# Performance work log

Measured on AMD Instinct MI355X. Metric: run time of the kernel, lower is better.

## Reference

```python
import jax, jax.numpy as jnp
import numpy as np

N = 4096
IN_F = 512
OUT_F = 256
HEADS = 4
HEAD_DIM = OUT_F // HEADS


def setup_inputs() -> dict:
    key = jax.random.key(0)
    k_feat, k_adj, k_w, k_a = jax.random.split(key, 4)
    features = jax.random.normal(k_feat, (N, IN_F), dtype=jnp.float32)
    adj_matrix = jax.random.uniform(k_adj, (N, N), dtype=jnp.float32)
    # xavier-uniform-ish init scaled small
    W = jax.random.normal(k_w, (OUT_F, IN_F), dtype=jnp.float32) * (1.0 / np.sqrt(IN_F))
    a = jax.random.normal(k_a, (HEADS, 2 * HEAD_DIM), dtype=jnp.float32) * 0.1
    bias = jnp.zeros((OUT_F,), dtype=jnp.float32)
    return {"features": features, "adj_matrix": adj_matrix, "W": W, "a": a, "bias": bias}


def reference(features, adj_matrix, W, a, bias):
    n = features.shape[0]
    h = features @ W.T                      # [N, OUT_F]
    hh = h.reshape(n, HEADS, HEAD_DIM)      # [N, H, D]
    # e[i,j,h] = leaky_relu(<h_i, a[:, :D]> + <h_j, a[:, D:]>) -- additive decomposition
    e_src = jnp.einsum('nhd,hd->nh', hh, a[:, :HEAD_DIM])   # [N, H]
    e_dst = jnp.einsum('nhd,hd->nh', hh, a[:, HEAD_DIM:])   # [N, H]
    e = e_src[:, None, :] + e_dst[None, :, :]               # [N, N, H]
    e = jnp.where(e >= 0, e, 0.2 * e)                       # leaky_relu(0.2)
    mask = adj_matrix[:, :, None] > 0.1                     # [N, N, 1]
    e = jnp.where(mask, e, -jnp.inf)
    attention = jax.nn.softmax(e, axis=1)                   # softmax over j
    attention = jnp.nan_to_num(attention, nan=0.0)          # fully-masked rows -> 0
    attention_mean = attention.mean(axis=2)                 # [N, N]
    h_out = attention_mean @ h + bias                       # [N, OUT_F]
    return h_out
```

## Files before the change

### kernel.cpp

```cpp
#include <hip/hip_runtime.h>
#include <math.h>

#define NN      4096
#define INF_    512
#define OUTF    256
#define NHEAD   4
#define HDIM    64
#define KSPLIT  16

typedef __attribute__((ext_vector_type(8))) short  short8x;
typedef __attribute__((ext_vector_type(4))) float  float4x;

__device__ __forceinline__ unsigned short f2bf(float x) {
    union { float f; unsigned int u; } c; c.f = x;
    unsigned int r = (c.u + 0x7FFFu + ((c.u >> 16) & 1u)) >> 16;
    return (unsigned short)r;
}
__device__ __forceinline__ float bflo(unsigned int u) {
    union { unsigned int x; float f; } c; c.x = u << 16; return c.f;
}
__device__ __forceinline__ float bfhi(unsigned int u) {
    union { unsigned int x; float f; } c; c.x = u & 0xFFFF0000u; return c.f;
}

__global__ __launch_bounds__(256) void k_cast(const float* __restrict__ feat,
                                              const float* __restrict__ W,
                                              unsigned short* __restrict__ featb,
                                              unsigned short* __restrict__ Wb) {
    const int b = blockIdx.x;
    const float* src;
    unsigned short* dst;
    int idx;
    if (b < 2048) { src = feat; dst = featb; idx = b * 1024 + threadIdx.x * 4; }
    else          { src = W;    dst = Wb;    idx = (b - 2048) * 1024 + threadIdx.x * 4; }
    float4x v = *(const float4x*)(src + idx);
    ushort4 u;
    u.x = f2bf(v[0]); u.y = f2bf(v[1]); u.z = f2bf(v[2]); u.w = f2bf(v[3]);
    *(ushort4*)(dst + idx) = u;
}

__global__ __launch_bounds__(256) void k_hedge(const unsigned short* __restrict__ featb,
                                               const unsigned short* __restrict__ Wb,
                                               const float* __restrict__ a,
                                               unsigned short* __restrict__ hT,
                                               float* __restrict__ es,
                                               unsigned short* __restrict__ Bt,
                                               unsigned short* __restrict__ Dt) {
    __shared__ __align__(16) unsigned short lds_f[16 * 40];
    __shared__ __align__(16) unsigned short lds_w[256 * 40];
    const int tid  = threadIdx.x;
    const int w    = tid >> 6;
    const int lane = tid & 63;
    const int lidx = lane & 15;
    const int quad = lane >> 4;
    const int i0   = blockIdx.x * 16;
    const int fr = (tid & 127) >> 3;
    const int fk = (tid & 7) * 4;
    const int wr = tid >> 3;
    const int wk = (tid & 7) * 4;

    float4x acc[4];
    #pragma unroll
    for (int nt = 0; nt < 4; ++nt) acc[nt] = (float4x){0.f, 0.f, 0.f, 0.f};

    ushort4 pf{0,0,0,0};
    ushort4 pw[8];
    if (tid < 128)
        pf = *(const ushort4*)&featb[(size_t)(i0 + fr) * INF_ + fk];
    #pragma unroll
    for (int it = 0; it < 8; ++it)
        pw[it] = *(const ushort4*)&Wb[(size_t)(it * 32 + wr) * INF_ + wk];

    for (int kt = 0; kt < INF_; kt += 32) {
        __syncthreads();
        if (tid < 128)
            *(ushort4*)&lds_f[fr * 40 + fk] = pf;
        #pragma unroll
        for (int it = 0; it < 8; ++it)
            *(ushort4*)&lds_w[(it * 32 + wr) * 40 + wk] = pw[it];
        __syncthreads();
        if (kt + 32 < INF_) {
            const int kn = kt + 32;
            if (tid < 128)
                pf = *(const ushort4*)&featb[(size_t)(i0 + fr) * INF_ + kn + fk];
            #pragma unroll
            for (int it = 0; it < 8; ++it)
                pw[it] = *(const ushort4*)&Wb[(size_t)(it * 32 + wr) * INF_ + kn + wk];
        }
        short8x af = *(const short8x*)&lds_f[lidx * 40 + quad * 8];
        short8x bw[4];
        #pragma unroll
        for (int nt = 0; nt < 4; ++nt)
            bw[nt] = *(const short8x*)&lds_w[(w * 64 + nt * 16 + lidx) * 40 + quad * 8];
        #pragma unroll
        for (int nt = 0; nt < 4; ++nt)
            acc[nt] = __builtin_amdgcn_mfma_f32_16x16x32_bf16(af, bw[nt], acc[nt], 0, 0, 0);
    }
    #pragma unroll
    for (int nt = 0; nt < 4; ++nt) {
        int col = w * 64 + nt * 16 + lidx;
        int m0r = i0 + quad * 4;
        ushort4 u;
        u.x = f2bf(acc[nt][0]); u.y = f2bf(acc[nt][1]);
        u.z = f2bf(acc[nt][2]); u.w = f2bf(acc[nt][3]);
        *(ushort4*)&hT[(size_t)col * NN + m0r] = u;
    }
    float asrc[4], adst[4];
    #pragma unroll
    for (int nt = 0; nt < 4; ++nt) {
        asrc[nt] = a[w * 2 * HDIM + nt * 16 + lidx];
        adst[nt] = a[w * 2 * HDIM + HDIM + nt * 16 + lidx];
    }
    #pragma unroll
    for (int r = 0; r < 4; ++r) {
        float s = 0.f, d = 0.f;
        #pragma unroll
        for (int nt = 0; nt < 4; ++nt) {
            s += acc[nt][r] * asrc[nt];
            d += acc[nt][r] * adst[nt];
        }
        #pragma unroll
        for (int off = 1; off < 16; off <<= 1) {
            s += __shfl_xor(s, off);
            d += __shfl_xor(d, off);
        }
        if (lidx == 0) {
            int row = i0 + quad * 4 + r;
            es[row * NHEAD + w] = s;
            Bt[row * NHEAD + w] = f2bf(__expf(d));
            Dt[row * NHEAD + w] = f2bf(__expf(0.2f * d));
        }
    }
}

__global__ __launch_bounds__(256) void k_attn(const float* __restrict__ adj,
                                              const float* __restrict__ es,
                                              const unsigned short* __restrict__ Bt,
                                              const unsigned short* __restrict__ Dt,
                                              unsigned short* __restrict__ attn) {
    __shared__ float red[4][8];
    __shared__ float cfs[8];
    const int tid = threadIdx.x;
    const int wv  = tid >> 6;
    const int lane = tid & 63;
    const int i = blockIdx.x;

    const float4x esv = ((const float4x*)es)[i];
    float TB[4];
    #pragma unroll
    for (int h = 0; h < 4; ++h) TB[h] = __expf(-esv[h]);
    const float4x* arow4 = (const float4x*)(adj + (size_t)i * NN);
    const uint4* B4 = (const uint4*)Bt;
    const uint4* D4 = (const uint4*)Dt;

    float4x av[4];
    float S1[4] = {0.f, 0.f, 0.f, 0.f};
    float S2[4] = {0.f, 0.f, 0.f, 0.f};
    #pragma unroll
    for (int t = 0; t < 4; ++t) {
        int jv = t * 256 + tid;
        av[t] = arow4[jv];
        uint4 bu0 = B4[jv * 2], bu1 = B4[jv * 2 + 1];
        uint4 du0 = D4[jv * 2], du1 = D4[jv * 2 + 1];
        unsigned int bwv[8] = {bu0.x, bu0.y, bu0.z, bu0.w, bu1.x, bu1.y, bu1.z, bu1.w};
        unsigned int dwv[8] = {du0.x, du0.y, du0.z, du0.w, du1.x, du1.y, du1.z, du1.w};
        #pragma unroll
        for (int u = 0; u < 4; ++u) {
            bool m = av[t][u] > 0.1f;
            float b0 = bflo(bwv[u * 2]), b1 = bfhi(bwv[u * 2]);
            float b2 = bflo(bwv[u * 2 + 1]), b3 = bfhi(bwv[u * 2 + 1]);
            float d0 = bflo(dwv[u * 2]), d1 = bfhi(dwv[u * 2]);
            float d2 = bflo(dwv[u * 2 + 1]), d3 = bfhi(dwv[u * 2 + 1]);
            bool p0 = b0 >= TB[0], p1 = b1 >= TB[1], p2 = b2 >= TB[2], p3 = b3 >= TB[3];
            S1[0] += (m && p0) ? b0 : 0.f;   S2[0] += (m && !p0) ? d0 : 0.f;
            S1[1] += (m && p1) ? b1 : 0.f;   S2[1] += (m && !p1) ? d1 : 0.f;
            S1[2] += (m && p2) ? b2 : 0.f;   S2[2] += (m && !p2) ? d2 : 0.f;
            S1[3] += (m && p3) ? b3 : 0.f;   S2[3] += (m && !p3) ? d3 : 0.f;
        }
    }
    #pragma unroll
    for (int off = 1; off < 64; off <<= 1) {
        #pragma unroll
        for (int h = 0; h < 4; ++h) {
            S1[h] += __shfl_xor(S1[h], off);
            S2[h] += __shfl_xor(S2[h], off);
        }
    }
    if (lane == 0) {
        #pragma unroll
        for (int h = 0; h < 4; ++h) { red[wv][h] = S1[h]; red[wv][4 + h] = S2[h]; }
    }
    __syncthreads();
    if (tid < 8)
        cfs[tid] = red[0][tid] + red[1][tid] + red[2][tid] + red[3][tid];
    __syncthreads();
    float cA[4], cC[4];
    #pragma unroll
    for (int h = 0; h < 4; ++h) {
        float A = __expf(esv[h]), C = __expf(0.2f * esv[h]);
        float den = A * cfs[h] + C * cfs[4 + h];
        float sc = den > 0.f ? 0.25f / den : 0.f;
        cA[h] = A * sc;
        cC[h] = C * sc;
    }

    unsigned short* orow = attn + (size_t)i * NN;
    #pragma unroll
    for (int t = 0; t < 4; ++t) {
        int jv = t * 256 + tid;
        uint4 bu0 = B4[jv * 2], bu1 = B4[jv * 2 + 1];
        uint4 du0 = D4[jv * 2], du1 = D4[jv * 2 + 1];
        unsigned int bwv[8] = {bu0.x, bu0.y, bu0.z, bu0.w, bu1.x, bu1.y, bu1.z, bu1.w};
        unsigned int dwv[8] = {du0.x, du0.y, du0.z, du0.w, du1.x, du1.y, du1.z, du1.w};
        ushort4 o;
        unsigned short* op = (unsigned short*)&o;
        #pragma unroll
        for (int u = 0; u < 4; ++u) {
            float b0 = bflo(bwv[u * 2]), b1 = bfhi(bwv[u * 2]);
            float b2 = bflo(bwv[u * 2 + 1]), b3 = bfhi(bwv[u * 2 + 1]);
            float d0 = bflo(dwv[u * 2]), d1 = bfhi(dwv[u * 2]);
            float d2 = bflo(dwv[u * 2 + 1]), d3 = bfhi(dwv[u * 2 + 1]);
            float p;
            p  = (b0 >= TB[0]) ? cA[0] * b0 : cC[0] * d0;
            p += (b1 >= TB[1]) ? cA[1] * b1 : cC[1] * d1;
            p += (b2 >= TB[2]) ? cA[2] * b2 : cC[2] * d2;
            p += (b3 >= TB[3]) ? cA[3] * b3 : cC[3] * d3;
            op[u] = f2bf((av[t][u] > 0.1f) ? p : 0.f);
        }
        *(ushort4*)&orow[jv * 4] = o;
    }
}

__global__ __launch_bounds__(256) void k_out_gemm(const unsigned short* __restrict__ attn,
                                                  const unsigned short* __restrict__ hT,
                                                  float* __restrict__ partials) {
    __shared__ __align__(16) unsigned short lds_a[64 * 40];
    __shared__ __align__(16) unsigned short lds_h[256 * 40];
    const int tid  = threadIdx.x;
    const int w    = tid >> 6;
    const int lane = tid & 63;
    const int lidx = lane & 15;
    const int quad = lane >> 4;
    const int i0    = blockIdx.x * 64;
    const int kbase = blockIdx.y * (NN / KSPLIT);
    const int srow = tid >> 3;
    const int skq  = tid & 7;

    float4x acc[4][4];
    #pragma unroll
    for (int p = 0; p < 4; ++p)
        #pragma unroll
        for (int q = 0; q < 4; ++q)
            acc[p][q] = (float4x){0.f, 0.f, 0.f, 0.f};

    ushort4 pa[2], ph[8];
    #pragma unroll
    for (int it = 0; it < 2; ++it)
        pa[it] = *(const ushort4*)&attn[(size_t)(i0 + it * 32 + srow) * NN + kbase + skq * 4];
    #pragma unroll
    for (int it = 0; it < 8; ++it)
        ph[it] = *(const ushort4*)&hT[(size_t)(it * 32 + srow) * NN + kbase + skq * 4];

    const int KSTEPS = (NN / KSPLIT) / 32;
    for (int ks = 0; ks < KSTEPS; ++ks) {
        __syncthreads();
        #pragma unroll
        for (int it = 0; it < 2; ++it)
            *(ushort4*)&lds_a[(it * 32 + srow) * 40 + skq * 4] = pa[it];
        #pragma unroll
        for (int it = 0; it < 8; ++it)
            *(ushort4*)&lds_h[(it * 32 + srow) * 40 + skq * 4] = ph[it];
        __syncthreads();
        if (ks < KSTEPS - 1) {
            const int ktn = kbase + (ks + 1) * 32;
            #pragma unroll
            for (int it = 0; it < 2; ++it)
                pa[it] = *(const ushort4*)&attn[(size_t)(i0 + it * 32 + srow) * NN + ktn + skq * 4];
            #pragma unroll
            for (int it = 0; it < 8; ++it)
                ph[it] = *(const ushort4*)&hT[(size_t)(it * 32 + srow) * NN + ktn + skq * 4];
        }
        short8x af[4], bfr[4];
        #pragma unroll
        for (int t = 0; t < 4; ++t) {
            af[t]  = *(const short8x*)&lds_a[(t * 16 + lidx) * 40 + quad * 8];
            bfr[t] = *(const short8x*)&lds_h[(w * 64 + t * 16 + lidx) * 40 + quad * 8];
        }
        #pragma unroll
        for (int it = 0; it < 4; ++it)
            #pragma unroll
            for (int nt = 0; nt < 4; ++nt)
                acc[it][nt] = __builtin_amdgcn_mfma_f32_16x16x32_bf16(
                    af[it], bfr[nt], acc[it][nt], 0, 0, 0);
    }
    float* pbase = partials + (size_t)blockIdx.y * NN * OUTF;
    #pragma unroll
    for (int it = 0; it < 4; ++it)
        #pragma unroll
        for (int nt = 0; nt < 4; ++nt)
            #pragma unroll
            for (int rr = 0; rr < 4; ++rr) {
                int row = i0 + it * 16 + quad * 4 + rr;
                int col = w * 64 + nt * 16 + lidx;
                pbase[(size_t)row * OUTF + col] = acc[it][nt][rr];
            }
}

__global__ __launch_bounds__(256) void k_reduce_out(const float* __restrict__ partials,
                                                    const float* __restrict__ bias,
                                                    float* __restrict__ out) {
    const int i = blockIdx.x;
    const int n = threadIdx.x;
    float acc = bias[n];
    #pragma unroll
    for (int s = 0; s < KSPLIT; ++s)
        acc += partials[((size_t)s * NN + i) * OUTF + n];
    out[(size_t)i * OUTF + n] = acc;
}

extern "C" void kernel_launch(void* const* d_in, const int* in_sizes, int n_in,
                              void* d_out, int out_size, void* d_ws, size_t ws_size,
                              hipStream_t stream) {
    const float* feat = (const float*)d_in[0];
    const float* adj  = (const float*)d_in[1];
    const float* W    = (const float*)d_in[2];
    const float* a    = (const float*)d_in[3];
    const float* bias = (const float*)d_in[4];
    float* out = (float*)d_out;

    char* ws = (char*)d_ws;
    float*          es    = (float*)(ws + 0);
    unsigned short* Btb   = (unsigned short*)(ws + (64u << 10));
    unsigned short* Dtb   = (unsigned short*)(ws + (96u << 10));
    unsigned short* hT    = (unsigned short*)(ws + (256u << 10));
    unsigned short* attn  = (unsigned short*)(ws + (2560u << 10));
    unsigned short* featb = (unsigned short*)(ws + (2560u << 10));
    unsigned short* Wb    = (unsigned short*)(ws + (6656u << 10));
    float*          partials = (float*)(ws + (36864u << 10));

    k_cast      <<<2176,             256, 0, stream>>>(feat, W, featb, Wb);
    k_hedge     <<<256,              256, 0, stream>>>(featb, Wb, a, hT, es, Btb, Dtb);
    k_attn      <<<NN,               256, 0, stream>>>(adj, es, Btb, Dtb, attn);
    k_out_gemm  <<<dim3(64, KSPLIT), 256, 0, stream>>>(attn, hT, partials);
    k_reduce_out<<<NN,               256, 0, stream>>>(partials, bias, out);
}
```

Baseline: 184.8 us.

## Fuse attention-probability generation into output GEMM and replace branch with fmax

The attention kernel now only computes per-row softmax denominators and scale factors. The output GEMM recomputes the bf16 attention probabilities on the fly from adj, Bt/Dt and those scales, then stages them into LDS. This drops the write and re-read of the 32 MB bf16 attention matrix. The leaky-relu branch is rewritten as fmax(A*b, C*d), using exp monotonicity. The cost is that adj is read twice (once in k_den, once in the fused GEMM), and the GEMM main loop carries extra ALU work.

```diff
diff --git a/kernel.cpp b/kernel.cpp
--- a/kernel.cpp
+++ b/kernel.cpp
@@ -43,7 +43,8 @@
                                                const unsigned short* __restrict__ Wb,
                                                const float* __restrict__ a,
                                                unsigned short* __restrict__ hT,
-                                               float* __restrict__ es,
+                                               float* __restrict__ Ae,
+                                               float* __restrict__ Ce,
                                                unsigned short* __restrict__ Bt,
                                                unsigned short* __restrict__ Dt) {
     __shared__ __align__(16) unsigned short lds_f[16 * 40];
@@ -126,115 +127,82 @@
         }
         if (lidx == 0) {
             int row = i0 + quad * 4 + r;
-            es[row * NHEAD + w] = s;
+            Ae[row * NHEAD + w] = __expf(s);
+            Ce[row * NHEAD + w] = __expf(0.2f * s);
             Bt[row * NHEAD + w] = f2bf(__expf(d));
             Dt[row * NHEAD + w] = f2bf(__expf(0.2f * d));
         }
     }
 }
 
-__global__ __launch_bounds__(256) void k_attn(const float* __restrict__ adj,
-                                              const float* __restrict__ es,
-                                              const unsigned short* __restrict__ Bt,
-                                              const unsigned short* __restrict__ Dt,
-                                              unsigned short* __restrict__ attn) {
-    __shared__ float red[4][8];
-    __shared__ float cfs[8];
+__global__ __launch_bounds__(256) void k_den(const float* __restrict__ adj,
+                                             const float* __restrict__ Ae,
+                                             const float* __restrict__ Ce,
+                                             const unsigned short* __restrict__ Bt,
+                                             const unsigned short* __restrict__ Dt,
+                                             float* __restrict__ cA_,
+                                             float* __restrict__ cC_) {
+    __shared__ float red[4][4];
     const int tid = threadIdx.x;
     const int wv  = tid >> 6;
     const int lane = tid & 63;
     const int i = blockIdx.x;
 
-    const float4x esv = ((const float4x*)es)[i];
-    float TB[4];
-    #pragma unroll
-    for (int h = 0; h < 4; ++h) TB[h] = __expf(-esv[h]);
+    const float4x Av = ((const float4x*)Ae)[i];
+    const float4x Cv = ((const float4x*)Ce)[i];
     const float4x* arow4 = (const float4x*)(adj + (size_t)i * NN);
     const uint4* B4 = (const uint4*)Bt;
     const uint4* D4 = (const uint4*)Dt;
 
-    float4x av[4];
-    float S1[4] = {0.f, 0.f, 0.f, 0.f};
-    float S2[4] = {0.f, 0.f, 0.f, 0.f};
+    float S[4] = {0.f, 0.f, 0.f, 0.f};
     #pragma unroll
     for (int t = 0; t < 4; ++t) {
         int jv = t * 256 + tid;
-        av[t] = arow4[jv];
+        float4x av = arow4[jv];
         uint4 bu0 = B4[jv * 2], bu1 = B4[jv * 2 + 1];
         uint4 du0 = D4[jv * 2], du1 = D4[jv * 2 + 1];
         unsigned int bwv[8] = {bu0.x, bu0.y, bu0.z, bu0.w, bu1.x, bu1.y, bu1.z, bu1.w};
         unsigned int dwv[8] = {du0.x, du0.y, du0.z, du0.w, du1.x, du1.y, du1.z, du1.w};
         #pragma unroll
         for (int u = 0; u < 4; ++u) {
-            bool m = av[t][u] > 0.1f;
+            bool m = av[u] > 0.1f;
             float b0 = bflo(bwv[u * 2]), b1 = bfhi(bwv[u * 2]);
             float b2 = bflo(bwv[u * 2 + 1]), b3 = bfhi(bwv[u * 2 + 1]);
             float d0 = bflo(dwv[u * 2]), d1 = bfhi(dwv[u * 2]);
             float d2 = bflo(dwv[u * 2 + 1]), d3 = bfhi(dwv[u * 2 + 1]);
-            bool p0 = b0 >= TB[0], p1 = b1 >= TB[1], p2 = b2 >= TB[2], p3 = b3 >= TB[3];
-            S1[0] += (m && p0) ? b0 : 0.f;   S2[0] += (m && !p0) ? d0 : 0.f;
-            S1[1] += (m && p1) ? b1 : 0.f;   S2[1] += (m && !p1) ? d1 : 0.f;
-            S1[2] += (m && p2) ? b2 : 0.f;   S2[2] += (m && !p2) ? d2 : 0.f;
-            S1[3] += (m && p3) ? b3 : 0.f;   S2[3] += (m && !p3) ? d3 : 0.f;
+            S[0] += m ? fmaxf(Av[0] * b0, Cv[0] * d0) : 0.f;
+            S[1] += m ? fmaxf(Av[1] * b1, Cv[1] * d1) : 0.f;
+            S[2] += m ? fmaxf(Av[2] * b2, Cv[2] * d2) : 0.f;
+            S[3] += m ? fmaxf(Av[3] * b3, Cv[3] * d3) : 0.f;
         }
     }
     #pragma unroll
     for (int off = 1; off < 64; off <<= 1) {
         #pragma unroll
-        for (int h = 0; h < 4; ++h) {
-            S1[h] += __shfl_xor(S1[h], off);
-            S2[h] += __shfl_xor(S2[h], off);
-        }
+        for (int h = 0; h < 4; ++h)
+            S[h] += __shfl_xor(S[h], off);
     }
     if (lane == 0) {
         #pragma unroll
-        for (int h = 0; h < 4; ++h) { red[wv][h] = S1[h]; red[wv][4 + h] = S2[h]; }
+        for (int h = 0; h < 4; ++h) red[wv][h] = S[h];
     }
     __syncthreads();
-    if (tid < 8)
-        cfs[tid] = red[0][tid] + red[1][tid] + red[2][tid] + red[3][tid];
-    __syncthreads();
-    float cA[4], cC[4];
-    #pragma unroll
-    for (int h = 0; h < 4; ++h) {
-        float A = __expf(esv[h]), C = __expf(0.2f * esv[h]);
-        float den = A * cfs[h] + C * cfs[4 + h];
+    if (tid < 4) {
+        float den = red[0][tid] + red[1][tid] + red[2][tid] + red[3][tid];
         float sc = den > 0.f ? 0.25f / den : 0.f;
-        cA[h] = A * sc;
-        cC[h] = C * sc;
-    }
-
-    unsigned short* orow = attn + (size_t)i * NN;
-    #pragma unroll
-    for (int t = 0; t < 4; ++t) {
-        int jv = t * 256 + tid;
-        uint4 bu0 = B4[jv * 2], bu1 = B4[jv * 2 + 1];
-        uint4 du0 = D4[jv * 2], du1 = D4[jv * 2 + 1];
-        unsigned int bwv[8] = {bu0.x, bu0.y, bu0.z, bu0.w, bu1.x, bu1.y, bu1.z, bu1.w};
-        unsigned int dwv[8] = {du0.x, du0.y, du0.z, du0.w, du1.x, du1.y, du1.z, du1.w};
-        ushort4 o;
-        unsigned short* op = (unsigned short*)&o;
-        #pragma unroll
-        for (int u = 0; u < 4; ++u) {
-            float b0 = bflo(bwv[u * 2]), b1 = bfhi(bwv[u * 2]);
-            float b2 = bflo(bwv[u * 2 + 1]), b3 = bfhi(bwv[u * 2 + 1]);
-            float d0 = bflo(dwv[u * 2]), d1 = bfhi(dwv[u * 2]);
-            float d2 = bflo(dwv[u * 2 + 1]), d3 = bfhi(dwv[u * 2 + 1]);
-            float p;
-            p  = (b0 >= TB[0]) ? cA[0] * b0 : cC[0] * d0;
-            p += (b1 >= TB[1]) ? cA[1] * b1 : cC[1] * d1;
-            p += (b2 >= TB[2]) ? cA[2] * b2 : cC[2] * d2;
-            p += (b3 >= TB[3]) ? cA[3] * b3 : cC[3] * d3;
-            op[u] = f2bf((av[t][u] > 0.1f) ? p : 0.f);
-        }
-        *(ushort4*)&orow[jv * 4] = o;
-    }
-}
-
-__global__ __launch_bounds__(256) void k_out_gemm(const unsigned short* __restrict__ attn,
-                                                  const unsigned short* __restrict__ hT,
-                                                  float* __restrict__ partials) {
-    __shared__ __align__(16) unsigned short lds_a[64 * 40];
+        cA_[i * NHEAD + tid] = Av[tid] * sc;
+        cC_[i * NHEAD + tid] = Cv[tid] * sc;
+    }
+}
+
+__global__ __launch_bounds__(256) void k_fused(const float* __restrict__ adj,
+                                               const unsigned short* __restrict__ Bt,
+                                               const unsigned short* __restrict__ Dt,
+                                               const float* __restrict__ cA_,
+                                               const float* __restrict__ cC_,
+                                               const unsigned short* __restrict__ hT,
+                                               float* __restrict__ partials) {
+    __shared__ __align__(16) unsigned short lds_p[64 * 40];
     __shared__ __align__(16) unsigned short lds_h[256 * 40];
     const int tid  = threadIdx.x;
     const int w    = tid >> 6;
@@ -243,9 +211,17 @@
     const int quad = lane >> 4;
     const int i0    = blockIdx.x * 64;
     const int kbase = blockIdx.y * (NN / KSPLIT);
+    const int il = tid >> 2;
+    const int jg = (tid & 3) * 8;
     const int srow = tid >> 3;
     const int skq  = tid & 7;
 
+    const float4x cAv = ((const float4x*)cA_)[i0 + il];
+    const float4x cCv = ((const float4x*)cC_)[i0 + il];
+    const float* arow = adj + (size_t)(i0 + il) * NN + kbase + jg;
+    const uint4* B4 = (const uint4*)Bt;
+    const uint4* D4 = (const uint4*)Dt;
+
     float4x acc[4][4];
     #pragma unroll
     for (int p = 0; p < 4; ++p)
@@ -253,29 +229,61 @@
         for (int q = 0; q < 4; ++q)
             acc[p][q] = (float4x){0.f, 0.f, 0.f, 0.f};
 
-    ushort4 pa[2], ph[8];
-    #pragma unroll
-    for (int it = 0; it < 2; ++it)
-        pa[it] = *(const ushort4*)&attn[(size_t)(i0 + it * 32 + srow) * NN + kbase + skq * 4];
+    float4x ad0, ad1;
+    uint4 bu[4], du[4];
+    ushort4 ph[8];
+    ad0 = *(const float4x*)(arow);
+    ad1 = *(const float4x*)(arow + 4);
+    {
+        int jq = (kbase + jg) >> 1;
+        #pragma unroll
+        for (int p = 0; p < 4; ++p) { bu[p] = B4[jq + p]; du[p] = D4[jq + p]; }
+    }
     #pragma unroll
     for (int it = 0; it < 8; ++it)
         ph[it] = *(const ushort4*)&hT[(size_t)(it * 32 + srow) * NN + kbase + skq * 4];
 
     const int KSTEPS = (NN / KSPLIT) / 32;
     for (int ks = 0; ks < KSTEPS; ++ks) {
+        ushort4 o0, o1;
+        {
+            unsigned short* op0 = (unsigned short*)&o0;
+            unsigned short* op1 = (unsigned short*)&o1;
+            #pragma unroll
+            for (int u = 0; u < 8; ++u) {
+                const uint4& buu = bu[u >> 1];
+                const uint4& duu = du[u >> 1];
+                unsigned int bw0 = (u & 1) ? buu.z : buu.x;
+                unsigned int bw1 = (u & 1) ? buu.w : buu.y;
+                unsigned int dw0 = (u & 1) ? duu.z : duu.x;
+                unsigned int dw1 = (u & 1) ? duu.w : duu.y;
+                float b0 = bflo(bw0), b1 = bfhi(bw0), b2 = bflo(bw1), b3 = bfhi(bw1);
+                float d0 = bflo(dw0), d1 = bfhi(dw0), d2 = bflo(dw1), d3 = bfhi(dw1);
+                float p;
+                p  = fmaxf(cAv[0] * b0, cCv[0] * d0);
+                p += fmaxf(cAv[1] * b1, cCv[1] * d1);
+                p += fmaxf(cAv[2] * b2, cCv[2] * d2);
+                p += fmaxf(cAv[3] * b3, cCv[3] * d3);
+                float am = (u < 4) ? ad0[u] : ad1[u - 4];
+                unsigned short r = f2bf((am > 0.1f) ? p : 0.f);
+                if (u < 4) op0[u] = r; else op1[u - 4] = r;
+            }
+        }
         __syncthreads();
-        #pragma unroll
-        for (int it = 0; it < 2; ++it)
-            *(ushort4*)&lds_a[(it * 32 + srow) * 40 + skq * 4] = pa[it];
+        *(ushort4*)&lds_p[il * 40 + jg]     = o0;
+        *(ushort4*)&lds_p[il * 40 + jg + 4] = o1;
         #pragma unroll
         for (int it = 0; it < 8; ++it)
             *(ushort4*)&lds_h[(it * 32 + srow) * 40 + skq * 4] = ph[it];
         __syncthreads();
         if (ks < KSTEPS - 1) {
+            const float* ap = arow + (ks + 1) * 32;
+            ad0 = *(const float4x*)(ap);
+            ad1 = *(const float4x*)(ap + 4);
+            int jq = (kbase + (ks + 1) * 32 + jg) >> 1;
+            #pragma unroll
+            for (int p = 0; p < 4; ++p) { bu[p] = B4[jq + p]; du[p] = D4[jq + p]; }
             const int ktn = kbase + (ks + 1) * 32;
-            #pragma unroll
-            for (int it = 0; it < 2; ++it)
-                pa[it] = *(const ushort4*)&attn[(size_t)(i0 + it * 32 + srow) * NN + ktn + skq * 4];
             #pragma unroll
             for (int it = 0; it < 8; ++it)
                 ph[it] = *(const ushort4*)&hT[(size_t)(it * 32 + srow) * NN + ktn + skq * 4];
@@ -283,7 +291,7 @@
         short8x af[4], bfr[4];
         #pragma unroll
         for (int t = 0; t < 4; ++t) {
-            af[t]  = *(const short8x*)&lds_a[(t * 16 + lidx) * 40 + quad * 8];
+            af[t]  = *(const short8x*)&lds_p[(t * 16 + lidx) * 40 + quad * 8];
             bfr[t] = *(const short8x*)&lds_h[(w * 64 + t * 16 + lidx) * 40 + quad * 8];
         }
         #pragma unroll
@@ -329,18 +337,20 @@
     float* out = (float*)d_out;
 
     char* ws = (char*)d_ws;
-    float*          es    = (float*)(ws + 0);
-    unsigned short* Btb   = (unsigned short*)(ws + (64u << 10));
-    unsigned short* Dtb   = (unsigned short*)(ws + (96u << 10));
-    unsigned short* hT    = (unsigned short*)(ws + (256u << 10));
-    unsigned short* attn  = (unsigned short*)(ws + (2560u << 10));
+    float*          Aeb   = (float*)(ws + 0);
+    float*          Ceb   = (float*)(ws + (64u << 10));
+    unsigned short* Btb   = (unsigned short*)(ws + (128u << 10));
+    unsigned short* Dtb   = (unsigned short*)(ws + (160u << 10));
+    float*          cAb   = (float*)(ws + (192u << 10));
+    float*          cCb   = (float*)(ws + (256u << 10));
+    unsigned short* hT    = (unsigned short*)(ws + (512u << 10));
     unsigned short* featb = (unsigned short*)(ws + (2560u << 10));
     unsigned short* Wb    = (unsigned short*)(ws + (6656u << 10));
-    float*          partials = (float*)(ws + (36864u << 10));
+    float*          partials = (float*)(ws + (8192u << 10));
 
     k_cast      <<<2176,             256, 0, stream>>>(feat, W, featb, Wb);
-    k_hedge     <<<256,              256, 0, stream>>>(featb, Wb, a, hT, es, Btb, Dtb);
-    k_attn      <<<NN,               256, 0, stream>>>(adj, es, Btb, Dtb, attn);
-    k_out_gemm  <<<dim3(64, KSPLIT), 256, 0, stream>>>(attn, hT, partials);
+    k_hedge     <<<256,              256, 0, stream>>>(featb, Wb, a, hT, Aeb, Ceb, Btb, Dtb);
+    k_den       <<<NN,               256, 0, stream>>>(adj, Aeb, Ceb, Btb, Dtb, cAb, cCb);
+    k_fused     <<<dim3(64, KSPLIT), 256, 0, stream>>>(adj, Btb, Dtb, cAb, cCb, hT, partials);
     k_reduce_out<<<NN,               256, 0, stream>>>(partials, bias, out);
 }
```

Measured after the change: 193.8 us. 1.05x slower.
